# Performance work log

Measured on AMD Instinct MI355X. Metric: run time of the kernel, lower is better.

## Reference

```python
import jax, jax.numpy as jnp
import numpy as np

BATCH, SEQ, CHANNELS, KSIZE = 4, 4096, 2048, 4


def setup_inputs() -> dict:
    key = jax.random.key(0)
    kx, kw = jax.random.split(key)
    x = jax.random.normal(kx, (BATCH, SEQ, CHANNELS), dtype=jnp.float32)
    # flax param init: normal(stddev=0.02), shape (kernel_size, channels)
    kernel = jax.random.normal(kw, (KSIZE, CHANNELS), dtype=jnp.float32) * 0.02
    return {"x": x, "kernel": kernel}


def reference(x, kernel):
    # Causal depthwise short conv: y[:, t] = silu(sum_j kernel[j] * x[:, t - j])
    # (the scan's window * kernel[::-1] unrolls to exactly this), with zero
    # left-padding of K-1 steps standing in for cache=None -> zeros.
    B, T, C = x.shape
    K = kernel.shape[0]
    kf = kernel.astype(x.dtype)
    cache = jnp.zeros((B, K - 1, C), dtype=x.dtype)
    xp = jnp.concatenate([cache, x], axis=1)  # [B, T+K-1, C]
    # Small fixed loop over kernel taps (K=4), fully parallel over time.
    y = kf[0][None, None, :] * xp[:, K - 1 : K - 1 + T, :]
    for j in range(1, K):
        y = y + kf[j][None, None, :] * xp[:, K - 1 - j : K - 1 - j + T, :]
    y = jax.nn.silu(y)
    # next_cache after the scan = last K-1 inputs of the padded stream
    next_cache = xp[:, T:, :]  # [B, K-1, C]
    return y, next_cache
```

## Files before the change

### kernel.cpp

```cpp
#include <hip/hip_runtime.h>
#include <math.h>


#define B_   4
#define T_   4096
#define C_   2048
#define K_   4
#define C4_  (C_ / 4)
#define TT_  32

__global__ __launch_bounds__(C4_) void dwconv_silu_kernel(
    const float4* __restrict__ x,
    const float4* __restrict__ kern,
    float4* __restrict__ y)
{
    const int c4 = threadIdx.x;
    const int b  = blockIdx.y;
    const int t0 = blockIdx.x * TT_;

    const float4 k0 = kern[0 * C4_ + c4];
    const float4 k1 = kern[1 * C4_ + c4];
    const float4 k2 = kern[2 * C4_ + c4];
    const float4 k3 = kern[3 * C4_ + c4];

    const float4* xb = x + (size_t)b * T_ * C4_;
    float4*       yb = y + (size_t)b * T_ * C4_;

    float4 xm1, xm2, xm3;
    if (t0 == 0) {
        xm1 = make_float4(0.f, 0.f, 0.f, 0.f);
        xm2 = xm1;
        xm3 = xm1;
    } else {
        xm1 = xb[(size_t)(t0 - 1) * C4_ + c4];
        xm2 = xb[(size_t)(t0 - 2) * C4_ + c4];
        xm3 = xb[(size_t)(t0 - 3) * C4_ + c4];
    }

    #pragma unroll 4
    for (int i = 0; i < TT_; ++i) {
        const int t = t0 + i;
        const float4 x0 = xb[(size_t)t * C4_ + c4];

        float4 r;
        r.x = fmaf(k0.x, x0.x, fmaf(k1.x, xm1.x, fmaf(k2.x, xm2.x, k3.x * xm3.x)));
        r.y = fmaf(k0.y, x0.y, fmaf(k1.y, xm1.y, fmaf(k2.y, xm2.y, k3.y * xm3.y)));
        r.z = fmaf(k0.z, x0.z, fmaf(k1.z, xm1.z, fmaf(k2.z, xm2.z, k3.z * xm3.z)));
        r.w = fmaf(k0.w, x0.w, fmaf(k1.w, xm1.w, fmaf(k2.w, xm2.w, k3.w * xm3.w)));

        r.x = r.x / (1.f + expf(-r.x));
        r.y = r.y / (1.f + expf(-r.y));
        r.z = r.z / (1.f + expf(-r.z));
        r.w = r.w / (1.f + expf(-r.w));

        yb[(size_t)t * C4_ + c4] = r;

        xm3 = xm2;
        xm2 = xm1;
        xm1 = x0;
    }
}

__global__ __launch_bounds__(256) void cache_copy_kernel(
    const float4* __restrict__ x, float4* __restrict__ cache)
{
    const int i = blockIdx.x * blockDim.x + threadIdx.x;
    if (i >= B_ * (K_ - 1) * C4_) return;
    const int b  = i / ((K_ - 1) * C4_);
    const int rc = i % ((K_ - 1) * C4_);
    const int t  = T_ - (K_ - 1) + rc / C4_;
    const int c4 = rc % C4_;
    cache[i] = x[((size_t)b * T_ + t) * C4_ + c4];
}

extern "C" void kernel_launch(void* const* d_in, const int* in_sizes, int n_in,
                              void* d_out, int out_size, void* d_ws, size_t ws_size,
                              hipStream_t stream)
{
    const float4* x    = (const float4*)d_in[0];
    const float4* kern = (const float4*)d_in[1];
    float*        out  = (float*)d_out;

    float4* y     = (float4*)out;
    float4* cache = (float4*)(out + (size_t)B_ * T_ * C_);

    dim3 grid(T_ / TT_, B_);
    dim3 block(C4_);
    dwconv_silu_kernel<<<grid, block, 0, stream>>>(x, kern, y);

    const int cache_elems4 = B_ * (K_ - 1) * C4_;
    cache_copy_kernel<<<(cache_elems4 + 255) / 256, 256, 0, stream>>>(x, cache);
}
```

Baseline: 242.6 us.

## Flatten conv to one thread per element, fuse cache copy, use fast silu

Replaces the time-tiled sliding-window kernel with a flat grid where each thread computes one float4 output and reloads its three previous timesteps, relying on cache hits instead of register reuse. The separate next_cache copy kernel is folded into the main kernel, which removes one launch. SiLU now uses __expf and a reciprocal instead of expf and a divide, and outputs go out through nontemporal stores. In exchange, global load instructions per output roughly quadruple and the fast exp slightly changes numerics.

```diff
diff --git a/kernel.cpp b/kernel.cpp
--- a/kernel.cpp
+++ b/kernel.cpp
@@ -7,70 +7,60 @@
 #define C_   2048
 #define K_   4
 #define C4_  (C_ / 4)
-#define TT_  32
 
-__global__ __launch_bounds__(C4_) void dwconv_silu_kernel(
+typedef float nat_float4 __attribute__((ext_vector_type(4)));
+
+__device__ __forceinline__ float silu_f(float v) {
+    return v * __frcp_rn(1.f + __expf(-v));
+}
+
+__device__ __forceinline__ void store_nt(float4* p, const float4& v) {
+    nat_float4 nv = { v.x, v.y, v.z, v.w };
+    __builtin_nontemporal_store(nv, reinterpret_cast<nat_float4*>(p));
+}
+
+__global__ __launch_bounds__(256) void dwconv_silu_flat(
     const float4* __restrict__ x,
     const float4* __restrict__ kern,
-    float4* __restrict__ y)
+    float4* __restrict__ y,
+    float4* __restrict__ cache)
 {
-    const int c4 = threadIdx.x;
-    const int b  = blockIdx.y;
-    const int t0 = blockIdx.x * TT_;
+    const int i  = blockIdx.x * 256 + threadIdx.x;
+    const int c4 = i & (C4_ - 1);
+    const int t  = (i >> 9) & (T_ - 1);
+    const int b  = i >> 21;
+
+    const float4 zero = make_float4(0.f, 0.f, 0.f, 0.f);
+
+    float4 x0, x1, x2, x3;
+    x0 = x[i];
+    if (t >= 3) {
+        x1 = x[i - 1 * C4_];
+        x2 = x[i - 2 * C4_];
+        x3 = x[i - 3 * C4_];
+    } else {
+        x1 = (t >= 1) ? x[i - 1 * C4_] : zero;
+        x2 = (t >= 2) ? x[i - 2 * C4_] : zero;
+        x3 = zero;
+    }
 
     const float4 k0 = kern[0 * C4_ + c4];
     const float4 k1 = kern[1 * C4_ + c4];
     const float4 k2 = kern[2 * C4_ + c4];
     const float4 k3 = kern[3 * C4_ + c4];
 
-    const float4* xb = x + (size_t)b * T_ * C4_;
-    float4*       yb = y + (size_t)b * T_ * C4_;
+    float4 r;
+    r.x = fmaf(k0.x, x0.x, fmaf(k1.x, x1.x, fmaf(k2.x, x2.x, k3.x * x3.x)));
+    r.y = fmaf(k0.y, x0.y, fmaf(k1.y, x1.y, fmaf(k2.y, x2.y, k3.y * x3.y)));
+    r.z = fmaf(k0.z, x0.z, fmaf(k1.z, x1.z, fmaf(k2.z, x2.z, k3.z * x3.z)));
+    r.w = fmaf(k0.w, x0.w, fmaf(k1.w, x1.w, fmaf(k2.w, x2.w, k3.w * x3.w)));
+    r.x = silu_f(r.x); r.y = silu_f(r.y); r.z = silu_f(r.z); r.w = silu_f(r.w);
 
-    float4 xm1, xm2, xm3;
-    if (t0 == 0) {
-        xm1 = make_float4(0.f, 0.f, 0.f, 0.f);
-        xm2 = xm1;
-        xm3 = xm1;
-    } else {
-        xm1 = xb[(size_t)(t0 - 1) * C4_ + c4];
-        xm2 = xb[(size_t)(t0 - 2) * C4_ + c4];
-        xm3 = xb[(size_t)(t0 - 3) * C4_ + c4];
+    store_nt(&y[i], r);
+
+    if (t >= T_ - 3) {
+        cache[((size_t)b * 3 + (t - (T_ - 3))) * C4_ + c4] = x0;
     }
-
-    #pragma unroll 4
-    for (int i = 0; i < TT_; ++i) {
-        const int t = t0 + i;
-        const float4 x0 = xb[(size_t)t * C4_ + c4];
-
-        float4 r;
-        r.x = fmaf(k0.x, x0.x, fmaf(k1.x, xm1.x, fmaf(k2.x, xm2.x, k3.x * xm3.x)));
-        r.y = fmaf(k0.y, x0.y, fmaf(k1.y, xm1.y, fmaf(k2.y, xm2.y, k3.y * xm3.y)));
-        r.z = fmaf(k0.z, x0.z, fmaf(k1.z, xm1.z, fmaf(k2.z, xm2.z, k3.z * xm3.z)));
-        r.w = fmaf(k0.w, x0.w, fmaf(k1.w, xm1.w, fmaf(k2.w, xm2.w, k3.w * xm3.w)));
-
-        r.x = r.x / (1.f + expf(-r.x));
-        r.y = r.y / (1.f + expf(-r.y));
-        r.z = r.z / (1.f + expf(-r.z));
-        r.w = r.w / (1.f + expf(-r.w));
-
-        yb[(size_t)t * C4_ + c4] = r;
-
-        xm3 = xm2;
-        xm2 = xm1;
-        xm1 = x0;
-    }
-}
-
-__global__ __launch_bounds__(256) void cache_copy_kernel(
-    const float4* __restrict__ x, float4* __restrict__ cache)
-{
-    const int i = blockIdx.x * blockDim.x + threadIdx.x;
-    if (i >= B_ * (K_ - 1) * C4_) return;
-    const int b  = i / ((K_ - 1) * C4_);
-    const int rc = i % ((K_ - 1) * C4_);
-    const int t  = T_ - (K_ - 1) + rc / C4_;
-    const int c4 = rc % C4_;
-    cache[i] = x[((size_t)b * T_ + t) * C4_ + c4];
 }
 
 extern "C" void kernel_launch(void* const* d_in, const int* in_sizes, int n_in,
@@ -84,10 +74,6 @@
     float4* y     = (float4*)out;
     float4* cache = (float4*)(out + (size_t)B_ * T_ * C_);
 
-    dim3 grid(T_ / TT_, B_);
-    dim3 block(C4_);
-    dwconv_silu_kernel<<<grid, block, 0, stream>>>(x, kern, y);
-
-    const int cache_elems4 = B_ * (K_ - 1) * C4_;
-    cache_copy_kernel<<<(cache_elems4 + 255) / 256, 256, 0, stream>>>(x, cache);
+    const int total = B_ * T_ * C4_;
+    dwconv_silu_flat<<<total / 256, 256, 0, stream>>>(x, kern, y, cache);
 }
```

Result: slower. 299.5 us (+23.4%).
